# Optimization experiments

Measured on AMD Instinct MI355X. Metric: run time of the kernel, lower is better.

The kernel has to match this reference:

```python
import jax, jax.numpy as jnp
import numpy as np

B, C, W, H = 16, 256, 32, 32
HEADS = 4


def setup_inputs() -> dict:
    key = jax.random.key(0)
    ks = jax.random.split(key, 9)
    d = C // HEADS
    return {
        "x": jax.random.normal(ks[0], (B, C, W, H), jnp.float32),
        "Wq": jax.random.normal(ks[1], (C, C), jnp.float32) * 0.05,
        "bq": jax.random.normal(ks[2], (C,), jnp.float32) * 0.05,
        "Wk": jax.random.normal(ks[3], (C, C), jnp.float32) * 0.05,
        "bk": jax.random.normal(ks[4], (C,), jnp.float32) * 0.05,
        "Wv": jax.random.normal(ks[5], (C, C), jnp.float32) * 0.05,
        "bv": jax.random.normal(ks[6], (C,), jnp.float32) * 0.05,
        "rel_h": jax.random.normal(ks[7], (1, HEADS, d, 1, H), jnp.float32),
        "rel_w": jax.random.normal(ks[8], (1, HEADS, d, W, 1), jnp.float32),
    }


def reference(x, Wq, bq, Wk, bk, Wv, bv, rel_h, rel_w):
    b, c, w, h = x.shape
    heads = rel_h.shape[1]
    d = c // heads
    n = w * h  # sequence length = spatial positions
    xf = x.reshape(b, c, n)

    def proj(Wt, bt):
        # 1x1 conv == per-position linear over channels
        y = jnp.einsum('oc,bcn->bon', Wt, xf) + bt[None, :, None]
        return y.reshape(b, heads, d, n)

    q = proj(Wq, bq)
    k = proj(Wk, bk)
    v = proj(Wv, bv)

    # similarity = q^T k : [b, heads, n, n]
    sim = jnp.einsum('bhdi,bhdj->bhij', q, k)
    # relative position bias content term: rel^T q
    rel = (rel_h + rel_w).reshape(heads, d, n)  # broadcast-add then flatten spatial
    qpos = jnp.einsum('hdi,bhdj->bhij', rel, q)

    attn = jax.nn.softmax(sim + qpos, axis=-1)
    # out = v @ attn^T : [b, heads, d, n]
    out = jnp.einsum('bhdn,bhmn->bhdm', v, attn)
    return out.reshape(b, c, w, h)
```

## Files before the change

kernel.cpp:

```cpp
#include <hip/hip_runtime.h>

constexpr int Bb  = 16;
constexpr int Cch = 256;
constexpr int NH  = 4;
constexpr int Dh  = 64;
constexpr int Nn  = 1024;

typedef _Float16 f16;
typedef __attribute__((ext_vector_type(8))) _Float16 f16x8;
typedef __attribute__((ext_vector_type(4))) _Float16 f16x4;
typedef __attribute__((ext_vector_type(4))) float    f32x4;

__global__ __launch_bounds__(256) void prep_rel(
    const float* __restrict__ rel_h, const float* __restrict__ rel_w,
    f16* __restrict__ rel_t)
{
    const int idx0 = (blockIdx.x * 256 + threadIdx.x) * 4;
    const int d0 = idx0 & 63;
    const int n  = (idx0 >> 6) & (Nn - 1);
    const int h  = idx0 >> 16;
    f16x4 w;
    #pragma unroll
    for (int u = 0; u < 4; u++) {
        const int hd = h * 64 + d0 + u;
        w[u] = (f16)(rel_h[hd * 32 + (n & 31)] + rel_w[hd * 32 + (n >> 5)]);
    }
    *(f16x4*)&rel_t[idx0] = w;
}

__global__ __launch_bounds__(256) void gemm_qkv(
    const float* __restrict__ x,
    const float* __restrict__ Wq, const float* __restrict__ Wk,
    const float* __restrict__ Wv,
    const float* __restrict__ bq, const float* __restrict__ bk,
    const float* __restrict__ bv,
    f16* __restrict__ qt, f16* __restrict__ kt, f16* __restrict__ vb)
{
    const int bx   = blockIdx.x;
    const int y    = blockIdx.y;
    const int b    = blockIdx.z;
    const int p    = y >> 1;
    const int half = y & 1;

    constexpr int ST = 40;
    __shared__ f16   Wt[128 * ST];
    __shared__ f16   Xt[128 * ST];
    __shared__ float T [32 * 132];

    const int t    = threadIdx.x;
    const int wave = t >> 6;
    const int lane = t & 63;
    const int l16  = lane & 15;
    const int quad = lane >> 4;
    const int wm   = wave >> 1;
    const int wsd  = wave & 1;

    const float* Wsel = (p == 0) ? Wq : (p == 1) ? Wk : Wv;

    f32x4 acc[4][4];
    #pragma unroll
    for (int mi = 0; mi < 4; mi++)
        #pragma unroll
        for (int ni = 0; ni < 4; ni++) acc[mi][ni] = (f32x4){0.f, 0.f, 0.f, 0.f};

    for (int c0 = 0; c0 < 256; c0 += 32) {
        float4 wreg[4], xreg[4];
        #pragma unroll
        for (int rep = 0; rep < 4; rep++) {
            const int e  = t + rep * 256;
            const int r  = e >> 3;
            const int c4 = e & 7;
            wreg[rep] = *(const float4*)
                &Wsel[(size_t)(half * 128 + r) * 256 + c0 + c4 * 4];
            const int cc = e >> 5;
            const int n4 = e & 31;
            xreg[rep] = *(const float4*)
                &x[((size_t)b * Cch + c0 + cc) * Nn + bx * 128 + n4 * 4];
        }
        __syncthreads();

        #pragma unroll
        for (int rep = 0; rep < 4; rep++) {
            const int e  = t + rep * 256;
            const int r  = e >> 3;
            const int c4 = e & 7;
            f16x4 wv;
            wv.x = (f16)wreg[rep].x; wv.y = (f16)wreg[rep].y;
            wv.z = (f16)wreg[rep].z; wv.w = (f16)wreg[rep].w;
            *(f16x4*)&Wt[r * ST + c4 * 4] = wv;
            const int cc = e >> 5;
            const int n4 = e & 31;
            *(float4*)&T[cc * 132 + n4 * 4] = xreg[rep];
        }
        __syncthreads();

        #pragma unroll
        for (int rep = 0; rep < 2; rep++) {
            const int e  = t + rep * 256;
            const int nn = e & 127;
            const int c8 = e >> 7;
            f16x8 xv;
            #pragma unroll
            for (int u = 0; u < 8; u++)
                xv[u] = (f16)T[(c8 * 8 + u) * 132 + nn];
            *(f16x8*)&Xt[nn * ST + c8 * 8] = xv;
        }
        __syncthreads();

        const f16* tf = (p < 2) ? Wt : Xt;
        const f16* ts = (p < 2) ? Xt : Wt;
        f16x8 af[4], bf[4];
        #pragma unroll
        for (int mi = 0; mi < 4; mi++)
            af[mi] = *(const f16x8*)&tf[(wm * 64 + mi * 16 + l16) * ST + quad * 8];
        #pragma unroll
        for (int ni = 0; ni < 4; ni++)
            bf[ni] = *(const f16x8*)&ts[(wsd * 64 + ni * 16 + l16) * ST + quad * 8];
        #pragma unroll
        for (int mi = 0; mi < 4; mi++)
            #pragma unroll
            for (int ni = 0; ni < 4; ni++)
                acc[mi][ni] = __builtin_amdgcn_mfma_f32_16x16x32_f16(
                    af[mi], bf[ni], acc[mi][ni], 0, 0, 0);
    }

    if (p < 2) {
        f16* yt = (p == 0) ? qt : kt;
        const float* bg = (p == 0) ? bq : bk;
        #pragma unroll
        for (int mi = 0; mi < 4; mi++) {
            const int o_in = half * 128 + wm * 64 + mi * 16 + quad * 4;
            const float4 b4 = *(const float4*)&bg[o_in];
            const int h = o_in >> 6;
            const int d = o_in & 63;
            #pragma unroll
            for (int ni = 0; ni < 4; ni++) {
                const int n = bx * 128 + wsd * 64 + ni * 16 + l16;
                f16x4 w;
                w.x = (f16)(acc[mi][ni][0] + b4.x);
                w.y = (f16)(acc[mi][ni][1] + b4.y);
                w.z = (f16)(acc[mi][ni][2] + b4.z);
                w.w = (f16)(acc[mi][ni][3] + b4.w);
                *(f16x4*)&yt[(((size_t)b * NH + h) * Nn + n) * Dh + d] = w;
            }
        }
    } else {
        #pragma unroll
        for (int ni = 0; ni < 4; ni++) {
            const int c  = half * 128 + wsd * 64 + ni * 16 + l16;
            const float bs = bv[c];
            #pragma unroll
            for (int mi = 0; mi < 4; mi++) {
                const int n = bx * 128 + wm * 64 + mi * 16 + quad * 4;
                f16x4 w;
                w.x = (f16)(acc[mi][ni][0] + bs);
                w.y = (f16)(acc[mi][ni][1] + bs);
                w.z = (f16)(acc[mi][ni][2] + bs);
                w.w = (f16)(acc[mi][ni][3] + bs);
                *(f16x4*)&vb[((size_t)b * Cch + c) * Nn + n] = w;
            }
        }
    }
}

__global__ __launch_bounds__(512, 4) void attn_mfma(
    const f16* __restrict__ qt, const f16* __restrict__ kt,
    const f16* __restrict__ relt, const f16* __restrict__ vb,
    float* __restrict__ out)
{
    const int bid = blockIdx.x;
    const int bh  = bid & 63;
    const int i0  = (bid >> 6) * 128;
    const int h   = bh & 3;
    const int b   = bh >> 2;

    const f16* qtb = qt  + (size_t)bh * Nn * Dh;
    const f16* ktb = kt  + (size_t)bh * Nn * Dh;
    const f16* rlt = relt + (size_t)h * Nn * Dh;
    const f16* vbb = vb  + (size_t)(b * Cch + h * Dh) * Nn;

    __shared__ f16 Qa_s[128 * 128];
    __shared__ f16 Ka_s[64 * 128];
    __shared__ f16 v_s [64 * 64];
    __shared__ f16 Pt_s[128 * 64];

    const int t    = threadIdx.x;
    const int wave = t >> 6;
    const int lane = t & 63;
    const int l16  = lane & 15;
    const int quad = lane >> 4;

    #pragma unroll
    for (int rep = 0; rep < 4; rep++) {
        const int e   = t + rep * 512;
        const int row = e >> 4;
        const int c8  = e & 15;
        const f16* src = (c8 < 8)
            ? &qtb[(size_t)(i0 + row) * Dh + c8 * 8]
            : &rlt[(size_t)(i0 + row) * Dh + (c8 - 8) * 8];
        *(f16x8*)&Qa_s[(row << 7) + ((c8 ^ (row & 7)) << 3)] = *(const f16x8*)src;
    }
    __syncthreads();

    f16x8 af[4];
    {
        const int row = wave * 16 + l16;
        #pragma unroll
        for (int k = 0; k < 4; k++)
            af[k] = *(const f16x8*)
                &Qa_s[(row << 7) + ((((k << 2) + quad) ^ (row & 7)) << 3)];
    }

    f16x8 ones;
    #pragma unroll
    for (int u = 0; u < 8; u++) ones[u] = (f16)1.0f;

    f32x4 Of[4], Ol;
    float m_r[4];
    Ol = (f32x4){0.f, 0.f, 0.f, 0.f};
    #pragma unroll
    for (int ds = 0; ds < 4; ds++) Of[ds] = (f32x4){0.f, 0.f, 0.f, 0.f};
    #pragma unroll
    for (int r = 0; r < 4; r++) m_r[r] = -1e30f;

    for (int j0 = 0; j0 < Nn; j0 += 64) {
        f16x8 kreg[2], vreg;
        #pragma unroll
        for (int rep = 0; rep < 2; rep++) {
            const int e   = t + rep * 512;
            const int row = e >> 4;
            const int c8  = e & 15;
            const f16* src = (c8 < 8)
                ? &ktb[(size_t)(j0 + row) * Dh + c8 * 8]
                : &qtb[(size_t)(j0 + row) * Dh + (c8 - 8) * 8];
            kreg[rep] = *(const f16x8*)src;
        }
        {
            const int row = t >> 3;
            const int c8  = t & 7;
            vreg = *(const f16x8*)&vbb[(size_t)row * Nn + j0 + c8 * 8];
        }

        __syncthreads();
        #pragma unroll
        for (int rep = 0; rep < 2; rep++) {
            const int e   = t + rep * 512;
            const int row = e >> 4;
            const int c8  = e & 15;
            *(f16x8*)&Ka_s[(row << 7) + ((c8 ^ (row & 7)) << 3)] = kreg[rep];
        }
        {
            const int row = t >> 3;
            const int c8  = t & 7;
            *(f16x8*)&v_s[(row << 6) + ((c8 ^ (row & 7)) << 3)] = vreg;
        }
        __syncthreads();

        f32x4 Sf[4];
        #pragma unroll
        for (int js = 0; js < 4; js++) Sf[js] = (f32x4){0.f, 0.f, 0.f, 0.f};
        #pragma unroll
        for (int k = 0; k < 4; k++) {
            f16x8 bb[4];
            #pragma unroll
            for (int js = 0; js < 4; js++) {
                const int row = js * 16 + l16;
                bb[js] = *(const f16x8*)
                    &Ka_s[(row << 7) + ((((k << 2) + quad) ^ (row & 7)) << 3)];
            }
            #pragma unroll
            for (int js = 0; js < 4; js++)
                Sf[js] = __builtin_amdgcn_mfma_f32_16x16x32_f16(
                    af[k], bb[js], Sf[js], 0, 0, 0);
        }

        #pragma unroll
        for (int r = 0; r < 4; r++) {
            float tm = fmaxf(fmaxf(Sf[0][r], Sf[1][r]),
                             fmaxf(Sf[2][r], Sf[3][r]));
            tm = fmaxf(tm, __shfl_xor(tm, 1));
            tm = fmaxf(tm, __shfl_xor(tm, 2));
            tm = fmaxf(tm, __shfl_xor(tm, 4));
            tm = fmaxf(tm, __shfl_xor(tm, 8));
            const float mnew  = fmaxf(m_r[r], tm);
            const float alpha = __expf(m_r[r] - mnew);
            m_r[r] = mnew;

            const int row = wave * 16 + quad * 4 + r;
            const int rx  = row & 7;
            #pragma unroll
            for (int js = 0; js < 4; js++) {
                const float p = __expf(Sf[js][r] - mnew);
                const int col = js * 16 + l16;
                Pt_s[(row << 6) + (((col >> 3) ^ rx) << 3) + (col & 7)] = (f16)p;
            }
            #pragma unroll
            for (int ds = 0; ds < 4; ds++) Of[ds][r] *= alpha;
            Ol[r] *= alpha;
        }

        #pragma unroll
        for (int ks = 0; ks < 2; ks++) {
            const int prow = wave * 16 + l16;
            f16x8 pa = *(const f16x8*)
                &Pt_s[(prow << 6) + ((((ks << 2) + quad) ^ (prow & 7)) << 3)];
            #pragma unroll
            for (int ds = 0; ds < 4; ds++) {
                const int vrow = ds * 16 + l16;
                f16x8 vv = *(const f16x8*)
                    &v_s[(vrow << 6) + ((((ks << 2) + quad) ^ (vrow & 7)) << 3)];
                Of[ds] = __builtin_amdgcn_mfma_f32_16x16x32_f16(
                    pa, vv, Of[ds], 0, 0, 0);
            }
            Ol = __builtin_amdgcn_mfma_f32_16x16x32_f16(
                pa, ones, Ol, 0, 0, 0);
        }
    }

    #pragma unroll
    for (int r = 0; r < 4; r++) {
        const float inv = 1.0f / Ol[r];
        const int i = i0 + wave * 16 + quad * 4 + r;
        #pragma unroll
        for (int ds = 0; ds < 4; ds++) {
            const int d = ds * 16 + l16;
            out[((size_t)(b * Cch + h * Dh + d)) * Nn + i] = Of[ds][r] * inv;
        }
    }
}

extern "C" void kernel_launch(void* const* d_in, const int* in_sizes, int n_in,
                              void* d_out, int out_size, void* d_ws, size_t ws_size,
                              hipStream_t stream)
{
    const float* x     = (const float*)d_in[0];
    const float* Wq    = (const float*)d_in[1];
    const float* bq    = (const float*)d_in[2];
    const float* Wk    = (const float*)d_in[3];
    const float* bk    = (const float*)d_in[4];
    const float* Wv    = (const float*)d_in[5];
    const float* bv    = (const float*)d_in[6];
    const float* rel_h = (const float*)d_in[7];
    const float* rel_w = (const float*)d_in[8];

    f16* ws = (f16*)d_ws;
    const size_t SZQ = (size_t)Bb * NH * Nn * Dh;
    f16* qt   = ws;
    f16* kt   = ws + SZQ;
    f16* vbuf = ws + 2 * SZQ;
    f16* relt = ws + 3 * SZQ;

    prep_rel<<<dim3(256), 256, 0, stream>>>(rel_h, rel_w, relt);
    gemm_qkv<<<dim3(Nn / 128, 6, Bb), 256, 0, stream>>>(
        x, Wq, Wk, Wv, bq, bk, bv, qt, kt, vbuf);
    attn_mfma<<<dim3(512), 512, 0, stream>>>(
        qt, kt, relt, vbuf, (float*)d_out);
}
```

Measured before the change: 181.6 us.

## Fuse rel-bias prep into attention load and drop LDS transpose in QKV GEMM

Removes the separate prep_rel kernel and computes the rel_h+rel_w bias on the fly while staging Q into shared memory in the attention kernel. This saves a launch and a round trip of the bias through global memory. Separately, the QKV GEMM now loads x as per-thread columns of 8 channels straight into registers. That drops the float staging buffer and one barrier, but trades coalesced float4 loads for strided scalar loads.

```diff
diff --git a/kernel.cpp b/kernel.cpp
--- a/kernel.cpp
+++ b/kernel.cpp
@@ -10,23 +10,6 @@
 typedef __attribute__((ext_vector_type(8))) _Float16 f16x8;
 typedef __attribute__((ext_vector_type(4))) _Float16 f16x4;
 typedef __attribute__((ext_vector_type(4))) float    f32x4;
-
-__global__ __launch_bounds__(256) void prep_rel(
-    const float* __restrict__ rel_h, const float* __restrict__ rel_w,
-    f16* __restrict__ rel_t)
-{
-    const int idx0 = (blockIdx.x * 256 + threadIdx.x) * 4;
-    const int d0 = idx0 & 63;
-    const int n  = (idx0 >> 6) & (Nn - 1);
-    const int h  = idx0 >> 16;
-    f16x4 w;
-    #pragma unroll
-    for (int u = 0; u < 4; u++) {
-        const int hd = h * 64 + d0 + u;
-        w[u] = (f16)(rel_h[hd * 32 + (n & 31)] + rel_w[hd * 32 + (n >> 5)]);
-    }
-    *(f16x4*)&rel_t[idx0] = w;
-}
 
 __global__ __launch_bounds__(256) void gemm_qkv(
     const float* __restrict__ x,
@@ -43,9 +26,8 @@
     const int half = y & 1;
 
     constexpr int ST = 40;
-    __shared__ f16   Wt[128 * ST];
-    __shared__ f16   Xt[128 * ST];
-    __shared__ float T [32 * 132];
+    __shared__ f16 Wt[128 * ST];
+    __shared__ f16 Xt[128 * ST];
 
     const int t    = threadIdx.x;
     const int wave = t >> 6;
@@ -64,7 +46,8 @@
         for (int ni = 0; ni < 4; ni++) acc[mi][ni] = (f32x4){0.f, 0.f, 0.f, 0.f};
 
     for (int c0 = 0; c0 < 256; c0 += 32) {
-        float4 wreg[4], xreg[4];
+        float4 wreg[4];
+        float  xcol[2][8];
         #pragma unroll
         for (int rep = 0; rep < 4; rep++) {
             const int e  = t + rep * 256;
@@ -72,10 +55,16 @@
             const int c4 = e & 7;
             wreg[rep] = *(const float4*)
                 &Wsel[(size_t)(half * 128 + r) * 256 + c0 + c4 * 4];
-            const int cc = e >> 5;
-            const int n4 = e & 31;
-            xreg[rep] = *(const float4*)
-                &x[((size_t)b * Cch + c0 + cc) * Nn + bx * 128 + n4 * 4];
+        }
+        #pragma unroll
+        for (int rep = 0; rep < 2; rep++) {
+            const int e  = t + rep * 256;
+            const int nn = e & 127;
+            const int c8 = e >> 7;
+            #pragma unroll
+            for (int u = 0; u < 8; u++)
+                xcol[rep][u] = x[((size_t)b * Cch + c0 + c8 * 8 + u) * Nn
+                                 + bx * 128 + nn];
         }
         __syncthreads();
 
@@ -88,12 +77,7 @@
             wv.x = (f16)wreg[rep].x; wv.y = (f16)wreg[rep].y;
             wv.z = (f16)wreg[rep].z; wv.w = (f16)wreg[rep].w;
             *(f16x4*)&Wt[r * ST + c4 * 4] = wv;
-            const int cc = e >> 5;
-            const int n4 = e & 31;
-            *(float4*)&T[cc * 132 + n4 * 4] = xreg[rep];
-        }
-        __syncthreads();
-
+        }
         #pragma unroll
         for (int rep = 0; rep < 2; rep++) {
             const int e  = t + rep * 256;
@@ -101,8 +85,7 @@
             const int c8 = e >> 7;
             f16x8 xv;
             #pragma unroll
-            for (int u = 0; u < 8; u++)
-                xv[u] = (f16)T[(c8 * 8 + u) * 132 + nn];
+            for (int u = 0; u < 8; u++) xv[u] = (f16)xcol[rep][u];
             *(f16x8*)&Xt[nn * ST + c8 * 8] = xv;
         }
         __syncthreads();
@@ -165,8 +148,8 @@
 
 __global__ __launch_bounds__(512, 4) void attn_mfma(
     const f16* __restrict__ qt, const f16* __restrict__ kt,
-    const f16* __restrict__ relt, const f16* __restrict__ vb,
-    float* __restrict__ out)
+    const float* __restrict__ rel_h, const float* __restrict__ rel_w,
+    const f16* __restrict__ vb, float* __restrict__ out)
 {
     const int bid = blockIdx.x;
     const int bh  = bid & 63;
@@ -176,7 +159,6 @@
 
     const f16* qtb = qt  + (size_t)bh * Nn * Dh;
     const f16* ktb = kt  + (size_t)bh * Nn * Dh;
-    const f16* rlt = relt + (size_t)h * Nn * Dh;
     const f16* vbb = vb  + (size_t)(b * Cch + h * Dh) * Nn;
 
     __shared__ f16 Qa_s[128 * 128];
@@ -195,10 +177,20 @@
         const int e   = t + rep * 512;
         const int row = e >> 4;
         const int c8  = e & 15;
-        const f16* src = (c8 < 8)
-            ? &qtb[(size_t)(i0 + row) * Dh + c8 * 8]
-            : &rlt[(size_t)(i0 + row) * Dh + (c8 - 8) * 8];
-        *(f16x8*)&Qa_s[(row << 7) + ((c8 ^ (row & 7)) << 3)] = *(const f16x8*)src;
+        f16x8 val;
+        if (c8 < 8) {
+            val = *(const f16x8*)&qtb[(size_t)(i0 + row) * Dh + c8 * 8];
+        } else {
+            const int n  = i0 + row;
+            const int d0 = (c8 - 8) * 8;
+            #pragma unroll
+            for (int u = 0; u < 8; u++) {
+                const int hd = h * 64 + d0 + u;
+                val[u] = (f16)(rel_h[hd * 32 + (n & 31)] +
+                               rel_w[hd * 32 + (n >> 5)]);
+            }
+        }
+        *(f16x8*)&Qa_s[(row << 7) + ((c8 ^ (row & 7)) << 3)] = val;
     }
     __syncthreads();
 
@@ -348,11 +340,9 @@
     f16* qt   = ws;
     f16* kt   = ws + SZQ;
     f16* vbuf = ws + 2 * SZQ;
-    f16* relt = ws + 3 * SZQ;
-
-    prep_rel<<<dim3(256), 256, 0, stream>>>(rel_h, rel_w, relt);
+
     gemm_qkv<<<dim3(Nn / 128, 6, Bb), 256, 0, stream>>>(
         x, Wq, Wk, Wv, bq, bk, bv, qt, kt, vbuf);
     attn_mfma<<<dim3(512), 512, 0, stream>>>(
-        qt, kt, relt, vbuf, (float*)d_out);
+        qt, kt, rel_h, rel_w, vbuf, (float*)d_out);
 }
```

Result: faster. 165.8 us (-8.7%).
